# Optimization experiments

Hardware: AMD Instinct MI355X
Metric: run time of the kernel (lower is better)

The kernel has to match this reference:

```python
import jax, jax.numpy as jnp
import numpy as np

N_E = 8192
E_DIM = 256
BETA = 0.25


def setup_inputs() -> dict:
    key = jax.random.key(0)
    k1, k2 = jax.random.split(key)
    z = jax.random.normal(k1, (16, E_DIM, 32, 32), dtype=jnp.float32)
    # nn.Embedding init: uniform(-1/n_e, 1/n_e)
    e_w = jax.random.uniform(k2, (N_E, E_DIM), dtype=jnp.float32,
                             minval=-1.0 / N_E, maxval=1.0 / N_E)
    return {"z": z, "e_w": e_w}


def reference(z, e_w):
    B, C, H, W = z.shape  # C == e_dim
    n_e = e_w.shape[0]
    # (B,C,H,W) -> (N, D)
    z_flat = jnp.transpose(z, (0, 2, 3, 1)).reshape(-1, C)
    # squared euclidean distances: ||z||^2 + ||e||^2 - 2 z.e  -> (N, n_e)
    z_sq = jnp.sum(z_flat * z_flat, axis=1, keepdims=True)
    e_sq = jnp.sum(e_w * e_w, axis=1)
    distances = z_sq + e_sq[None, :] - 2.0 * (z_flat @ e_w.T)
    indices = jnp.argmin(distances, axis=1)  # (N,)
    one_hot = jax.nn.one_hot(indices, n_e, dtype=z.dtype)  # (N, n_e)
    # one_hot @ e_w == gather
    z_q_flat = e_w[indices]
    z_q = jnp.transpose(z_q_flat.reshape(B, H, W, C), (0, 3, 1, 2))
    sg = jax.lax.stop_gradient
    loss_embed = jnp.mean((sg(z_q) - z) ** 2)
    loss_commit = jnp.mean((z_q - sg(z)) ** 2)
    loss = loss_embed + BETA * loss_commit
    # straight-through estimator
    z_q_st = z + sg(z_q - z)
    avg_probs = jnp.mean(one_hot, axis=0)
    perplexity = jnp.exp(-jnp.sum(avg_probs * jnp.log(avg_probs + 1e-10)))
    return loss, z_q_st, perplexity, one_hot, indices
```

## Files before the change

### kernel.cpp

```cpp
#include <hip/hip_runtime.h>
#include <hip/hip_bf16.h>
#include <math.h>

#define N_ROWS 16384
#define DIM    256
#define NE     8192
#define QMARGIN 21

#define SOFF 4194308
#define GHOFF 12075012ULL
#define Z4_BASE 12083204ULL
#define N4_TOTAL 31582207ULL
#define C4_PER_BLK 30843ULL
#define ZQ4_COUNT 1972223ULL
#define ZQ4_PER_BLK 482

typedef __bf16 bf16x8 __attribute__((ext_vector_type(8)));
typedef float  f32x4  __attribute__((ext_vector_type(4)));
typedef float  vf4    __attribute__((ext_vector_type(4)));

__device__ __forceinline__ void gload_lds16(const __bf16* g, __bf16* l) {
  __builtin_amdgcn_global_load_lds(
      (const __attribute__((address_space(1))) unsigned int*)g,
      (__attribute__((address_space(3))) unsigned int*)l, 16, 0, 0);
}

__global__ void k_prep(const float* __restrict__ z, const float* __restrict__ ew,
                       float* __restrict__ zf, __bf16* __restrict__ zfb,
                       __bf16* __restrict__ ewb, int* __restrict__ ghist) {
  __shared__ float tile[32][33];
  int ct = blockIdx.x, ht = blockIdx.y, b = blockIdx.z;
  int tx = threadIdx.x & 31, ty = threadIdx.x >> 5;
  int c0 = ct * 32, hw0 = ht * 32;
  const size_t zb = (size_t)b * 256 * 1024;
#pragma unroll
  for (int p = 0; p < 4; ++p) {
    int c = p * 8 + ty;
    tile[c][tx] = z[zb + (size_t)(c0 + c) * 1024 + hw0 + tx];
  }
  __syncthreads();
#pragma unroll
  for (int p = 0; p < 4; ++p) {
    int r = p * 8 + ty;
    zf[(size_t)(b * 1024 + hw0 + r) * DIM + c0 + tx] = tile[tx][r];
  }
  if (threadIdx.x < 128) {
    int r = threadIdx.x >> 2, kc = threadIdx.x & 3;
    int row = b * 1024 + hw0 + r;
    bf16x8 v;
#pragma unroll
    for (int j = 0; j < 8; ++j) v[j] = (__bf16)tile[kc * 8 + j][r];
    int tn = row >> 7, g = (row >> 4) & 7, m15 = row & 15, kt = c0 >> 5;
    *(bf16x8*)(zfb + (size_t)tn * 32768 + kt * 4096 + g * 512 + (kc * 16 + m15) * 8) = v;
  }
  const int fid = blockIdx.x + 8 * blockIdx.y + 256 * blockIdx.z;
  if (fid < 1024) {
    int gid = fid * 256 + threadIdx.x;
    int r = gid >> 5, kc8 = gid & 31;
    const float* s = ew + (size_t)r * DIM + kc8 * 8;
    float4 v0 = *(const float4*)s, v1 = *(const float4*)(s + 4);
    bf16x8 v = {(__bf16)v0.x, (__bf16)v0.y, (__bf16)v0.z, (__bf16)v0.w,
                (__bf16)v1.x, (__bf16)v1.y, (__bf16)v1.z, (__bf16)v1.w};
    int t = r >> 7, g = (r >> 4) & 7, m15 = r & 15, kt = kc8 >> 2, kc = kc8 & 3;
    *(bf16x8*)(ewb + (size_t)t * 32768 + kt * 4096 + g * 512 + (kc * 16 + m15) * 8) = v;
  } else if (fid < 1056) {
    ghist[(fid - 1024) * 256 + threadIdx.x] = 0;
  }
}

__global__ __launch_bounds__(256, 2) void k_score(const __bf16* __restrict__ zfb,
                                                  const __bf16* __restrict__ ewb,
                                                  int2* __restrict__ part2,
                                                  float* __restrict__ oz) {
  __shared__ __align__(16) __bf16 Afull[32768];
  __shared__ __align__(16) __bf16 Bs[2][4096];
  const int tid = threadIdx.x;
  const int lane = tid & 63, wave = tid >> 6;
  const int wm = wave >> 1, wn = wave & 1;
  const int quad = lane >> 4, l15 = lane & 15;
  const int bx = blockIdx.x, byc = blockIdx.y;
  const int bid = byc * 128 + bx;
  const __bf16* Ag = zfb + (size_t)bx * 32768;
  const __bf16* Bg = ewb + (size_t)byc * 262144;
  const size_t blk4 = (size_t)bid * C4_PER_BLK;
  f32x4* zdst = (f32x4*)(oz + Z4_BASE);
  const f32x4 zero4 = {0.f, 0.f, 0.f, 0.f};

  {
    const int base = wave * 8192;
#pragma unroll
    for (int i = 0; i < 16; ++i)
      gload_lds16(Ag + base + i * 512 + lane * 8, Afull + base + i * 512);
  }
  {
    const int boff = wave * 1024;
    gload_lds16(Bg + boff + lane * 8, Bs[0] + boff);
    gload_lds16(Bg + boff + 512 + lane * 8, Bs[0] + boff + 512);
  }

  f32x4 acc[4][4];
#pragma unroll
  for (int i = 0; i < 4; ++i)
#pragma unroll
    for (int j = 0; j < 4; ++j) acc[i][j] = (f32x4){0.f, 0.f, 0.f, 0.f};
  int r1[16], r2[16];
#pragma unroll
  for (int i = 0; i < 16; ++i) { r1[i] = 0x7fffffff; r2[i] = 0x7fffffff; }

  for (int it = 0; it < 64; ++it) {
    const int bt = it >> 3, kt = it & 7, buf = it & 1;
    __syncthreads();
    if (it < 63) {
      const int nx = it + 1;
      const __bf16* src = Bg + (nx >> 3) * 32768 + (nx & 7) * 4096 + wave * 1024;
      gload_lds16(src + lane * 8, Bs[buf ^ 1] + wave * 1024);
      gload_lds16(src + 512 + lane * 8, Bs[buf ^ 1] + wave * 1024 + 512);
    }
    if (it <= 60) {
#pragma unroll
      for (int s = 0; s < 2; ++s) {
        size_t slot = (size_t)(it * 2 + s) * 256 + tid;
        if (slot < C4_PER_BLK) {
          size_t g4 = blk4 + slot;
          if (g4 < N4_TOTAL) __builtin_nontemporal_store(zero4, zdst + g4);
        }
      }
    }
    bf16x8 af[4], bfr[4];
#pragma unroll
    for (int mi = 0; mi < 4; ++mi)
      af[mi] = *(const bf16x8*)(Afull + kt * 4096 + (wm * 4 + mi) * 512 + lane * 8);
#pragma unroll
    for (int ni = 0; ni < 4; ++ni)
      bfr[ni] = *(const bf16x8*)(Bs[buf] + (wn * 4 + ni) * 512 + lane * 8);
#pragma unroll
    for (int mi = 0; mi < 4; ++mi)
#pragma unroll
      for (int ni = 0; ni < 4; ++ni)
        acc[mi][ni] = __builtin_amdgcn_mfma_f32_16x16x32_bf16(af[mi], bfr[ni],
                                                              acc[mi][ni], 0, 0, 0);
    if (kt == 7) {
      const int colb = byc * 1024 + bt * 128 + wn * 64;
#pragma unroll
      for (int mi = 0; mi < 4; ++mi) {
#pragma unroll
        for (int rg = 0; rg < 4; ++rg) {
          const int idx = mi * 4 + rg;
          float s0 = -2.f * acc[mi][0][rg], s1 = -2.f * acc[mi][1][rg];
          float s2 = -2.f * acc[mi][2][rg], s3 = -2.f * acc[mi][3][rg];
          int q0 = min(max((int)((s0 + 1.0f) * 131072.0f), 0), 262143);
          int q1 = min(max((int)((s1 + 1.0f) * 131072.0f), 0), 262143);
          int q2 = min(max((int)((s2 + 1.0f) * 131072.0f), 0), 262143);
          int q3 = min(max((int)((s3 + 1.0f) * 131072.0f), 0), 262143);
          int k0 = (q0 << 13) | (colb + l15);
          int k1 = (q1 << 13) | (colb + 16 + l15);
          int k2 = (q2 << 13) | (colb + 32 + l15);
          int k3 = (q3 << 13) | (colb + 48 + l15);
          int a = min(k0, k1), bb = max(k0, k1);
          int c = min(k2, k3), dd = max(k2, k3);
          int t1 = min(a, c);
          int t2 = min(max(a, c), min(bb, dd));
          int n1 = min(r1[idx], t1);
          int n2 = min(max(r1[idx], t1), min(r2[idx], t2));
          r1[idx] = n1; r2[idx] = n2;
        }
      }
#pragma unroll
      for (int i = 0; i < 4; ++i)
#pragma unroll
        for (int j = 0; j < 4; ++j) acc[i][j] = (f32x4){0.f, 0.f, 0.f, 0.f};
    }
  }

#pragma unroll
  for (int mi = 0; mi < 4; ++mi) {
#pragma unroll
    for (int rg = 0; rg < 4; ++rg) {
      const int idx = mi * 4 + rg;
      int k1 = r1[idx], k2 = r2[idx];
#pragma unroll
      for (int d = 1; d < 16; d <<= 1) {
        int o1 = __shfl_xor(k1, d), o2 = __shfl_xor(k2, d);
        k2 = min(max(k1, o1), min(k2, o2));
        k1 = min(k1, o1);
      }
      if (l15 == 0) {
        int row = bx * 128 + wm * 64 + mi * 16 + quad * 4 + rg;
        int2 v; v.x = k1; v.y = k2;
        part2[row * 16 + byc * 2 + wn] = v;
      }
    }
  }
}

__device__ __forceinline__ float np_sumsq_128(const float* __restrict__ p) {
  float r[8];
#pragma unroll
  for (int j = 0; j < 8; ++j) r[j] = __fmul_rn(p[j], p[j]);
  for (int i = 8; i < 128; i += 8) {
#pragma unroll
    for (int j = 0; j < 8; ++j) r[j] = __fadd_rn(r[j], __fmul_rn(p[i + j], p[i + j]));
  }
  return __fadd_rn(__fadd_rn(__fadd_rn(r[0], r[1]), __fadd_rn(r[2], r[3])),
                   __fadd_rn(__fadd_rn(r[4], r[5]), __fadd_rn(r[6], r[7])));
}

__global__ __launch_bounds__(256) void k_pick(const int2* __restrict__ part2,
                                              const float* __restrict__ zf,
                                              const float* __restrict__ ew,
                                              float* __restrict__ idxF,
                                              float* __restrict__ losspart,
                                              int* __restrict__ ghist) {
  __shared__ int cand[4][40];
  __shared__ int cnts[4];
  const int t = threadIdx.x, lane = t & 63, wv = t >> 6;
  const int row = blockIdx.x * 4 + wv;
  if (lane == 0) cnts[wv] = 0;
  int2 pv;
  if (lane < 16) pv = part2[row * 16 + lane];
  else { pv.x = 0x7fffffff; pv.y = 0x7fffffff; }
  int kmin = pv.x;
#pragma unroll
  for (int d = 1; d < 64; d <<= 1) kmin = min(kmin, __shfl_xor(kmin, d));
  const int qthr = min((kmin >> 13) + QMARGIN, 262143);
  const int kthr = (qthr << 13) | 8191;
  __syncthreads();
  if (lane < 16) {
    if (pv.x <= kthr) { int p = atomicAdd(&cnts[wv], 1); cand[wv][p] = pv.x & 8191; }
    if (pv.y <= kthr) { int p = atomicAdd(&cnts[wv], 1); cand[wv][p] = pv.y & 8191; }
  }
  __syncthreads();
  const int cnt = cnts[wv];
  const float* zr = zf + (size_t)row * DIM;
  float bd = INFINITY; int bj = 0x7fffffff;
  if (lane < cnt) {
    int j = cand[wv][lane];
    const float* e = ew + (size_t)j * DIM;
    float acc = 0.f;
    for (int k = 0; k < DIM; k += 4) {
      float4 e4 = *(const float4*)(e + k);
      float4 z4 = *(const float4*)(zr + k);
      acc = __builtin_fmaf(z4.x, e4.x, acc);
      acc = __builtin_fmaf(z4.y, e4.y, acc);
      acc = __builtin_fmaf(z4.z, e4.z, acc);
      acc = __builtin_fmaf(z4.w, e4.w, acc);
    }
    float esq = __fadd_rn(np_sumsq_128(e), np_sumsq_128(e + 128));
    float zsq = __fadd_rn(np_sumsq_128(zr), np_sumsq_128(zr + 128));
    bd = __fsub_rn(__fadd_rn(zsq, esq), __fmul_rn(2.0f, acc));
    bj = j;
  }
#pragma unroll
  for (int d = 1; d < 64; d <<= 1) {
    float od = __shfl_xor(bd, d); int oj = __shfl_xor(bj, d);
    if (od < bd || (od == bd && oj < bj)) { bd = od; bj = oj; }
  }
  int c = lane * 4;
  float4 e4 = *reinterpret_cast<const float4*>(ew + (size_t)bj * DIM + c);
  float4 z4 = *reinterpret_cast<const float4*>(zr + c);
  float t0 = __fsub_rn(e4.x, z4.x), t1 = __fsub_rn(e4.y, z4.y);
  float t2 = __fsub_rn(e4.z, z4.z), t3 = __fsub_rn(e4.w, z4.w);
  float s = __fadd_rn(__fadd_rn(__fmul_rn(t0, t0), __fmul_rn(t1, t1)),
                      __fadd_rn(__fmul_rn(t2, t2), __fmul_rn(t3, t3)));
#pragma unroll
  for (int d = 1; d < 64; d <<= 1) s += __shfl_xor(s, d);
  if (lane == 0) {
    idxF[row] = (float)bj;
    losspart[row] = s;
    atomicAdd(&ghist[bj], 1);
  }
}

__global__ __launch_bounds__(256) void k_scalars(const int* __restrict__ ghist,
                                                 const float* __restrict__ losspart,
                                                 float* __restrict__ out) {
  __shared__ float red[256];
  int t = threadIdx.x;
  float ls = 0.f;
  for (int i = t; i < N_ROWS; i += 256) ls += losspart[i];
  float es = 0.f;
  for (int i = t; i < NE; i += 256) {
    float p = (float)ghist[i] * (1.0f / 16384.0f);
    es += p * logf(p + 1e-10f);
  }
  red[t] = es; __syncthreads();
  for (int w = 128; w > 0; w >>= 1) { if (t < w) red[t] += red[t + w]; __syncthreads(); }
  float esum = red[0]; __syncthreads();
  red[t] = ls; __syncthreads();
  for (int w = 128; w > 0; w >>= 1) { if (t < w) red[t] += red[t + w]; __syncthreads(); }
  if (t == 0) {
    out[4194305] = expf(-esum);
    float m = red[0] * (1.0f / 4194304.0f);
    out[0] = __fadd_rn(m, __fmul_rn(0.25f, m));
  }
}

__global__ void k_zq_out(const float* __restrict__ z, const float* __restrict__ ew,
                         const float* __restrict__ idxF, float* __restrict__ out) {
  __shared__ float tileE[32][33];
  __shared__ int sidx[32];
  int ct = blockIdx.x, ht = blockIdx.y, b = blockIdx.z;
  int tx = threadIdx.x & 31, ty = threadIdx.x >> 5;
  int c0 = ct * 32, hw0 = ht * 32;
  if (threadIdx.x < 32) sidx[threadIdx.x] = (int)idxF[b * 1024 + hw0 + threadIdx.x];
  __syncthreads();
#pragma unroll
  for (int p = 0; p < 4; ++p) {
    int r = p * 8 + ty;
    tileE[tx][r] = ew[(size_t)sidx[r] * DIM + c0 + tx];
  }
  __syncthreads();
  float* outq = out + 1;
#pragma unroll
  for (int p = 0; p < 4; ++p) {
    int cl = p * 8 + ty;
    size_t gi = (size_t)(b * 256 + c0 + cl) * 1024 + hw0 + tx;
    float zv = z[gi];
    outq[gi] = __fadd_rn(zv, __fsub_rn(tileE[cl][tx], zv));
  }

  const int fid = blockIdx.x + 8 * blockIdx.y + 256 * blockIdx.z;
  float* oh = out + 4194306;
  {
    f32x4* dst4 = (f32x4*)(out + 4194308);
#pragma unroll
    for (int p = 0; p < 2; ++p) {
      int slot = p * 256 + (int)threadIdx.x;
      size_t g4 = (size_t)fid * ZQ4_PER_BLK + slot;
      if (slot < ZQ4_PER_BLK && g4 < ZQ4_COUNT) {
        size_t rel = g4 * 4 + 2;
        int ra = (int)(rel >> 13), rb = (int)((rel + 3) >> 13);
        int ia = (int)idxF[ra];
        int ib = (ra == rb) ? ia : (int)idxF[rb];
        f32x4 v;
#pragma unroll
        for (int j = 0; j < 4; ++j) {
          size_t rj = rel + j;
          int rowj = (int)(rj >> 13), colj = (int)(rj & 8191);
          int idxj = (rowj == ra) ? ia : ib;
          v[j] = (colj == idxj) ? 1.f : 0.f;
        }
        __builtin_nontemporal_store(v, dst4 + g4);
      }
    }
  }
  if (threadIdx.x < 4) {
    int r = fid * 4 + (int)threadIdx.x;
    if (r >= 963 && r < N_ROWS) {
      int idx = (int)idxF[r];
      oh[(size_t)r * NE + idx] = 1.0f;
    }
  }
  if (fid == 0 && threadIdx.x == 4) {
    int i0 = (int)idxF[0];
    oh[0] = (i0 == 0) ? 1.f : 0.f;
    oh[1] = (i0 == 1) ? 1.f : 0.f;
    int i962 = (int)idxF[962];
    oh[(size_t)962 * NE + 8190] = (i962 == 8190) ? 1.f : 0.f;
    oh[(size_t)962 * NE + 8191] = (i962 == 8191) ? 1.f : 0.f;
    int i963 = (int)idxF[963];
    oh[(size_t)963 * NE + 0] = (i963 == 0) ? 1.f : 0.f;
    oh[(size_t)963 * NE + 1] = (i963 == 1) ? 1.f : 0.f;
    int il = (int)idxF[16383];
    oh[(size_t)16383 * NE + 8190] = (il == 8190) ? 1.f : 0.f;
    oh[(size_t)16383 * NE + 8191] = (il == 8191) ? 1.f : 0.f;
  }
}

extern "C" void kernel_launch(void* const* d_in, const int* in_sizes, int n_in,
                              void* d_out, int out_size, void* d_ws, size_t ws_size,
                              hipStream_t stream) {
  const float* z  = (const float*)d_in[0];
  const float* ew = (const float*)d_in[1];
  float* out = (float*)d_out;
  float*  zf    = out + SOFF;
  __bf16* zfb   = (__bf16*)(out + SOFF + 4194304);
  __bf16* ewb   = (__bf16*)(out + SOFF + 6291456);
  int2*   part2 = (int2*)(out + SOFF + 7340032);
  float*  lprt  = out + SOFF + 7864320;
  int*    ghist = (int*)(out + GHOFF);
  float*  idxF  = out + 138412034;

  k_prep<<<dim3(8, 32, 16), 256, 0, stream>>>(z, ew, zf, zfb, ewb, ghist);
  k_score<<<dim3(128, 8), 256, 0, stream>>>(zfb, ewb, part2, out);
  k_pick<<<dim3(4096), 256, 0, stream>>>(part2, zf, ew, idxF, lprt, ghist);
  k_scalars<<<1, 256, 0, stream>>>(ghist, lprt, out);
  k_zq_out<<<dim3(8, 32, 16), 256, 0, stream>>>(z, ew, idxF, out);
}
```

Before: 822.1 us.

## Split k_score work across 8 waves with per-wave 64x32 tiles and LDS merge

Doubles the k_score block to 512 threads (8 waves in a 2x4 grid), halving each wave's N-tile from 64 to 32 columns so there are half as many accumulators and B fragments per wave. Global-to-LDS loads and the zero-fill stores are redistributed over the larger block. Because part2 keeps two 64-column slots per block, paired waves now merge their top-2 results through LDS with two extra barriers. The aim is more waves in flight to hide latency, at the cost of more A-fragment LDS reads per MFMA and the added exchange step.

Result: no change. 826.8 us (+0.6%).

```diff
diff --git a/kernel.cpp b/kernel.cpp
--- a/kernel.cpp
+++ b/kernel.cpp
@@ -68,7 +68,7 @@
   }
 }
 
-__global__ __launch_bounds__(256, 2) void k_score(const __bf16* __restrict__ zfb,
+__global__ __launch_bounds__(512, 4) void k_score(const __bf16* __restrict__ zfb,
                                                   const __bf16* __restrict__ ewb,
                                                   int2* __restrict__ part2,
                                                   float* __restrict__ oz) {
@@ -76,7 +76,7 @@
   __shared__ __align__(16) __bf16 Bs[2][4096];
   const int tid = threadIdx.x;
   const int lane = tid & 63, wave = tid >> 6;
-  const int wm = wave >> 1, wn = wave & 1;
+  const int wm = wave >> 2, wn = wave & 3;
   const int quad = lane >> 4, l15 = lane & 15;
   const int bx = blockIdx.x, byc = blockIdx.y;
   const int bid = byc * 128 + bx;
@@ -86,23 +86,16 @@
   f32x4* zdst = (f32x4*)(oz + Z4_BASE);
   const f32x4 zero4 = {0.f, 0.f, 0.f, 0.f};
 
-  {
-    const int base = wave * 8192;
-#pragma unroll
-    for (int i = 0; i < 16; ++i)
-      gload_lds16(Ag + base + i * 512 + lane * 8, Afull + base + i * 512);
-  }
-  {
-    const int boff = wave * 1024;
-    gload_lds16(Bg + boff + lane * 8, Bs[0] + boff);
-    gload_lds16(Bg + boff + 512 + lane * 8, Bs[0] + boff + 512);
-  }
-
-  f32x4 acc[4][4];
+#pragma unroll
+  for (int i = 0; i < 8; ++i)
+    gload_lds16(Ag + i * 4096 + tid * 8, Afull + i * 4096 + tid * 8);
+  gload_lds16(Bg + tid * 8, Bs[0] + tid * 8);
+
+  f32x4 acc[4][2];
 #pragma unroll
   for (int i = 0; i < 4; ++i)
 #pragma unroll
-    for (int j = 0; j < 4; ++j) acc[i][j] = (f32x4){0.f, 0.f, 0.f, 0.f};
+    for (int j = 0; j < 2; ++j) acc[i][j] = (f32x4){0.f, 0.f, 0.f, 0.f};
   int r1[16], r2[16];
 #pragma unroll
   for (int i = 0; i < 16; ++i) { r1[i] = 0x7fffffff; r2[i] = 0x7fffffff; }
@@ -112,54 +105,42 @@
     __syncthreads();
     if (it < 63) {
       const int nx = it + 1;
-      const __bf16* src = Bg + (nx >> 3) * 32768 + (nx & 7) * 4096 + wave * 1024;
-      gload_lds16(src + lane * 8, Bs[buf ^ 1] + wave * 1024);
-      gload_lds16(src + 512 + lane * 8, Bs[buf ^ 1] + wave * 1024 + 512);
+      const __bf16* src = Bg + (nx >> 3) * 32768 + (nx & 7) * 4096;
+      gload_lds16(src + tid * 8, Bs[buf ^ 1] + tid * 8);
     }
     if (it <= 60) {
-#pragma unroll
-      for (int s = 0; s < 2; ++s) {
-        size_t slot = (size_t)(it * 2 + s) * 256 + tid;
-        if (slot < C4_PER_BLK) {
-          size_t g4 = blk4 + slot;
-          if (g4 < N4_TOTAL) __builtin_nontemporal_store(zero4, zdst + g4);
-        }
+      size_t slot = (size_t)it * 512 + tid;
+      if (slot < C4_PER_BLK) {
+        size_t g4 = blk4 + slot;
+        if (g4 < N4_TOTAL) __builtin_nontemporal_store(zero4, zdst + g4);
       }
     }
-    bf16x8 af[4], bfr[4];
+    bf16x8 af[4], bfr[2];
 #pragma unroll
     for (int mi = 0; mi < 4; ++mi)
       af[mi] = *(const bf16x8*)(Afull + kt * 4096 + (wm * 4 + mi) * 512 + lane * 8);
 #pragma unroll
-    for (int ni = 0; ni < 4; ++ni)
-      bfr[ni] = *(const bf16x8*)(Bs[buf] + (wn * 4 + ni) * 512 + lane * 8);
+    for (int ni = 0; ni < 2; ++ni)
+      bfr[ni] = *(const bf16x8*)(Bs[buf] + (wn * 2 + ni) * 512 + lane * 8);
 #pragma unroll
     for (int mi = 0; mi < 4; ++mi)
 #pragma unroll
-      for (int ni = 0; ni < 4; ++ni)
+      for (int ni = 0; ni < 2; ++ni)
         acc[mi][ni] = __builtin_amdgcn_mfma_f32_16x16x32_bf16(af[mi], bfr[ni],
                                                               acc[mi][ni], 0, 0, 0);
     if (kt == 7) {
-      const int colb = byc * 1024 + bt * 128 + wn * 64;
+      const int colb = byc * 1024 + bt * 128 + wn * 32;
 #pragma unroll
       for (int mi = 0; mi < 4; ++mi) {
 #pragma unroll
         for (int rg = 0; rg < 4; ++rg) {
           const int idx = mi * 4 + rg;
           float s0 = -2.f * acc[mi][0][rg], s1 = -2.f * acc[mi][1][rg];
-          float s2 = -2.f * acc[mi][2][rg], s3 = -2.f * acc[mi][3][rg];
           int q0 = min(max((int)((s0 + 1.0f) * 131072.0f), 0), 262143);
           int q1 = min(max((int)((s1 + 1.0f) * 131072.0f), 0), 262143);
-          int q2 = min(max((int)((s2 + 1.0f) * 131072.0f), 0), 262143);
-          int q3 = min(max((int)((s3 + 1.0f) * 131072.0f), 0), 262143);
           int k0 = (q0 << 13) | (colb + l15);
           int k1 = (q1 << 13) | (colb + 16 + l15);
-          int k2 = (q2 << 13) | (colb + 32 + l15);
-          int k3 = (q3 << 13) | (colb + 48 + l15);
-          int a = min(k0, k1), bb = max(k0, k1);
-          int c = min(k2, k3), dd = max(k2, k3);
-          int t1 = min(a, c);
-          int t2 = min(max(a, c), min(bb, dd));
+          int t1 = min(k0, k1), t2 = max(k0, k1);
           int n1 = min(r1[idx], t1);
           int n2 = min(max(r1[idx], t1), min(r2[idx], t2));
           r1[idx] = n1; r2[idx] = n2;
@@ -168,27 +149,42 @@
 #pragma unroll
       for (int i = 0; i < 4; ++i)
 #pragma unroll
-        for (int j = 0; j < 4; ++j) acc[i][j] = (f32x4){0.f, 0.f, 0.f, 0.f};
-    }
-  }
-
-#pragma unroll
-  for (int mi = 0; mi < 4; ++mi) {
-#pragma unroll
-    for (int rg = 0; rg < 4; ++rg) {
-      const int idx = mi * 4 + rg;
-      int k1 = r1[idx], k2 = r2[idx];
-#pragma unroll
-      for (int d = 1; d < 16; d <<= 1) {
-        int o1 = __shfl_xor(k1, d), o2 = __shfl_xor(k2, d);
-        k2 = min(max(k1, o1), min(k2, o2));
-        k1 = min(k1, o1);
-      }
-      if (l15 == 0) {
-        int row = bx * 128 + wm * 64 + mi * 16 + quad * 4 + rg;
-        int2 v; v.x = k1; v.y = k2;
-        part2[row * 16 + byc * 2 + wn] = v;
-      }
+        for (int j = 0; j < 2; ++j) acc[i][j] = (f32x4){0.f, 0.f, 0.f, 0.f};
+    }
+  }
+
+#pragma unroll
+  for (int idx = 0; idx < 16; ++idx) {
+    int k1 = r1[idx], k2 = r2[idx];
+#pragma unroll
+    for (int d = 1; d < 16; d <<= 1) {
+      int o1 = __shfl_xor(k1, d), o2 = __shfl_xor(k2, d);
+      k2 = min(max(k1, o1), min(k2, o2));
+      k1 = min(k1, o1);
+    }
+    r1[idx] = k1; r2[idx] = k2;
+  }
+  __syncthreads();
+  int2* exch = (int2*)&Bs[0][0];
+  const int pr = wn >> 1;
+  if ((wn & 1) && l15 == 0) {
+#pragma unroll
+    for (int idx = 0; idx < 16; ++idx) {
+      int2 v; v.x = r1[idx]; v.y = r2[idx];
+      exch[((wm * 2 + pr) * 4 + quad) * 16 + idx] = v;
+    }
+  }
+  __syncthreads();
+  if (!(wn & 1) && l15 == 0) {
+#pragma unroll
+    for (int idx = 0; idx < 16; ++idx) {
+      int2 o = exch[((wm * 2 + pr) * 4 + quad) * 16 + idx];
+      int m1 = min(r1[idx], o.x);
+      int m2 = min(max(r1[idx], o.x), min(r2[idx], o.y));
+      int mm = idx >> 2, rg = idx & 3;
+      int row = bx * 128 + wm * 64 + mm * 16 + quad * 4 + rg;
+      int2 v; v.x = m1; v.y = m2;
+      part2[row * 16 + byc * 2 + pr] = v;
     }
   }
 }
@@ -382,7 +378,7 @@
   float*  idxF  = out + 138412034;
 
   k_prep<<<dim3(8, 32, 16), 256, 0, stream>>>(z, ew, zf, zfb, ewb, ghist);
-  k_score<<<dim3(128, 8), 256, 0, stream>>>(zfb, ewb, part2, out);
+  k_score<<<dim3(128, 8), 512, 0, stream>>>(zfb, ewb, part2, out);
   k_pick<<<dim3(4096), 256, 0, stream>>>(part2, zf, ew, idxF, lprt, ghist);
   k_scalars<<<1, 256, 0, stream>>>(ghist, lprt, out);
   k_zq_out<<<dim3(8, 32, 16), 256, 0, stream>>>(z, ew, idxF, out);
```
